# Performance work log

Measured on AMD Instinct MI355X. Metric: run time of the kernel, lower is better.

The kernel has to match this reference:

```python
import jax, jax.numpy as jnp
import numpy as np

D_MODEL = 1024
N_HEADS = 16
D_K = D_MODEL // N_HEADS
D_FF = 4096
EPS = 1e-5


def _layer_norm(x, gamma, beta):
    mu = jnp.mean(x, axis=-1, keepdims=True)
    var = jnp.var(x, axis=-1, keepdims=True)
    return (x - mu) * jax.lax.rsqrt(var + EPS) * gamma + beta


def setup_inputs() -> dict:
    key = jax.random.key(0)
    ks = jax.random.split(key, 16)
    s = 1.0 / np.sqrt(D_MODEL)
    sf = 1.0 / np.sqrt(D_FF)
    return {
        "x": jax.random.normal(ks[0], (2, 2048, D_MODEL), dtype=jnp.float32),
        "Wq": jax.random.uniform(ks[1], (D_MODEL, D_MODEL), minval=-s, maxval=s),
        "bq": jax.random.uniform(ks[2], (D_MODEL,), minval=-s, maxval=s),
        "Wk": jax.random.uniform(ks[3], (D_MODEL, D_MODEL), minval=-s, maxval=s),
        "bk": jax.random.uniform(ks[4], (D_MODEL,), minval=-s, maxval=s),
        "Wv": jax.random.uniform(ks[5], (D_MODEL, D_MODEL), minval=-s, maxval=s),
        "bv": jax.random.uniform(ks[6], (D_MODEL,), minval=-s, maxval=s),
        "Wo": jax.random.uniform(ks[7], (D_MODEL, D_MODEL), minval=-s, maxval=s),
        "bo": jax.random.uniform(ks[8], (D_MODEL,), minval=-s, maxval=s),
        "W1": jax.random.uniform(ks[9], (D_MODEL, D_FF), minval=-s, maxval=s),
        "b1": jax.random.uniform(ks[10], (D_FF,), minval=-s, maxval=s),
        "W2": jax.random.uniform(ks[11], (D_FF, D_MODEL), minval=-sf, maxval=sf),
        "b2": jax.random.uniform(ks[12], (D_MODEL,), minval=-sf, maxval=sf),
        "g1": jnp.ones((D_MODEL,)),
        "be1": jnp.zeros((D_MODEL,)),
        "g2": jnp.ones((D_MODEL,)),
        "be2": jnp.zeros((D_MODEL,)),
    }


def reference(x, Wq, bq, Wk, bk, Wv, bv, Wo, bo, W1, b1, W2, b2, g1, be1, g2, be2):
    B, S, _ = x.shape

    def heads(y):  # (B,S,D) -> (B,H,S,dk)
        return y.reshape(B, S, N_HEADS, D_K).transpose(0, 2, 1, 3)

    q = heads(x @ Wq + bq)
    k = heads(x @ Wk + bk)
    v = heads(x @ Wv + bv)

    scores = jnp.einsum("bhqd,bhkd->bhqk", q, k) / np.sqrt(D_K)
    attn = jax.nn.softmax(scores, axis=-1)
    out = jnp.einsum("bhqk,bhkd->bhqd", attn, v)
    out = out.transpose(0, 2, 1, 3).reshape(B, S, D_MODEL)
    attn_out = out @ Wo + bo

    resid_mid = _layer_norm(x + attn_out, g1, be1)
    ff = jnp.maximum(resid_mid @ W1 + b1, 0.0) @ W2 + b2
    return _layer_norm(resid_mid + ff, g2, be2)
```

## Files before the change

### kernel.cpp

```cpp
#include <hip/hip_runtime.h>

#define DM   1024
#define DFF  4096
#define NH   16
#define DKH  64
#define SEQ  2048
#define BATCH 2
#define ROWS (BATCH*SEQ)
#define QKS  2048

typedef __bf16 bf16x8 __attribute__((ext_vector_type(8)));
typedef float  f32x4  __attribute__((ext_vector_type(4)));

__device__ __forceinline__ unsigned short f2b(float f) {
    unsigned int u = __builtin_bit_cast(unsigned int, f);
    u += 0x7fffu + ((u >> 16) & 1u);
    return (unsigned short)(u >> 16);
}
__device__ __forceinline__ float b2f(unsigned short u) {
    return __builtin_bit_cast(float, (unsigned int)u << 16);
}
__device__ __forceinline__ float exp2_raw(float x) {
    float r;
    asm("v_exp_f32 %0, %1" : "=v"(r) : "v"(x));
    return r;
}

__device__ __forceinline__ void gl_lds16(const unsigned short* g, unsigned short* l) {
    __builtin_amdgcn_global_load_lds(
        (const __attribute__((address_space(1))) unsigned int*)(const void*)g,
        (__attribute__((address_space(3))) unsigned int*)(void*)l, 16, 0, 0);
}

__global__ __launch_bounds__(256) void k_prep(const float* __restrict__ x,
                                              const float* __restrict__ Wq,
                                              const float* __restrict__ Wk,
                                              const float* __restrict__ Wv,
                                              const float* __restrict__ Wo,
                                              const float* __restrict__ W1,
                                              const float* __restrict__ W2,
                                              unsigned short* __restrict__ xb,
                                              unsigned short* __restrict__ WqkT,
                                              unsigned short* __restrict__ WvT,
                                              unsigned short* __restrict__ WoT,
                                              unsigned short* __restrict__ W1T,
                                              unsigned short* __restrict__ W2T) {
    int z = blockIdx.z;
    int bid = blockIdx.y * gridDim.x + blockIdx.x;
    int tx = threadIdx.x, ty = threadIdx.y;
    if (z == 6) {
        int i = bid * 256 + ty * 32 + tx;
        float4 v = ((const float4*)x)[i];
        ushort4 u;
        u.x = f2b(v.x); u.y = f2b(v.y); u.z = f2b(v.z); u.w = f2b(v.w);
        ((ushort4*)xb)[i] = u;
        return;
    }
    const float* W; unsigned short* WT; int R, C;
    if      (z == 0) { W = Wq; WT = WqkT;                     R = DM;  C = DM;  }
    else if (z == 1) { W = Wk; WT = WqkT + (size_t)DM * DM;   R = DM;  C = DM;  }
    else if (z == 2) { W = Wv; WT = WvT;                      R = DM;  C = DM;  }
    else if (z == 3) { W = Wo; WT = WoT;                      R = DM;  C = DM;  }
    else if (z == 4) { W = W1; WT = W1T;                      R = DM;  C = DFF; }
    else             { W = W2; WT = W2T;                      R = DFF; C = DM;  }
    int ct = C / 32;
    if (bid >= (R / 32) * ct) return;
    int c0 = (bid % ct) * 32, r0 = (bid / ct) * 32;
    __shared__ float t[32][33];
#pragma unroll
    for (int i = 0; i < 4; i++) {
        int r = ty + i * 8;
        t[r][tx] = W[(size_t)(r0 + r) * C + c0 + tx];
    }
    __syncthreads();
#pragma unroll
    for (int i = 0; i < 4; i++) {
        int r = ty + i * 8;
        WT[(size_t)(c0 + r) * R + r0 + tx] = f2b(t[tx][r]);
    }
}

template<int WM, int WN, bool OUTF32, bool RELU, bool BIASROW, bool VPERM, bool SCALE2, bool SPLITK, bool SUPER2D>
__global__ __launch_bounds__(256) void k_gemm_bt(const unsigned short* __restrict__ A,
                                                 const unsigned short* __restrict__ BT,
                                                 const float* __restrict__ bias,
                                                 const float* __restrict__ bias2,
                                                 int bsplit, float sc2,
                                                 void* __restrict__ Cout,
                                                 int M, int N, int K) {
    constexpr int BM = 2 * WM, BN = 2 * WN;
    constexpr int MT = WM / 16, NT = WN / 16;
    constexpr int IA = BM / 32, IB = BN / 32;
    __shared__ unsigned short As[BM][64] __attribute__((aligned(16)));
    __shared__ unsigned short Bs[BN][64] __attribute__((aligned(16)));
    int tid = threadIdx.x;
    int w = tid >> 6, l = tid & 63;
    int wr = w >> 1, wc = w & 1;
    int l15 = l & 15, lg = l >> 4;

    int bid = blockIdx.y * gridDim.x + blockIdx.x;
    int nwg = gridDim.x * gridDim.y;
    int m0, n0;
    if (SUPER2D) {
        int xcd = bid & 7, q = bid >> 3;
        int RM = gridDim.y >> 1, RN = gridDim.x >> 2;
        int mI = (xcd >> 2) * RM + (q % RM);
        int nI = (xcd & 3) * RN + (q / RM);
        m0 = mI * BM; n0 = nI * BN;
    } else {
        int swz = (bid & 7) * (nwg >> 3) + (bid >> 3);
        m0 = (swz / gridDim.x) * BM; n0 = (swz % gridDim.x) * BN;
    }

    int kb_ = SPLITK ? (int)blockIdx.z * (K >> 1) : 0;
    int Keff = SPLITK ? (K >> 1) : K;

    int lr8 = l >> 3;
    int gsrc = (l & 7) ^ lr8;
    const unsigned short* Abase = A  + (size_t)(m0 + w * (BM / 4) + lr8) * K + kb_ + gsrc * 8;
    const unsigned short* Bbase = BT + (size_t)(n0 + w * (BN / 4) + lr8) * K + kb_ + gsrc * 8;

    f32x4 acc[MT][NT] = {};

    int nk = Keff >> 6;
    for (int kt = 0; kt < nk; ++kt) {
        __syncthreads();
#pragma unroll
        for (int it = 0; it < IA; ++it)
            gl_lds16(Abase + (size_t)(it * 8) * K + kt * 64, &As[w * (BM / 4) + it * 8][0]);
#pragma unroll
        for (int it = 0; it < IB; ++it)
            gl_lds16(Bbase + (size_t)(it * 8) * K + kt * 64, &Bs[w * (BN / 4) + it * 8][0]);
        __syncthreads();
#pragma unroll
        for (int ks = 0; ks < 2; ++ks) {
            int glog = ks * 4 + lg;
            bf16x8 af[MT], bfr[NT];
#pragma unroll
            for (int mt = 0; mt < MT; ++mt) {
                int row = wr * WM + mt * 16 + l15;
                af[mt] = *(const bf16x8*)&As[row][(glog ^ (row & 7)) << 3];
            }
#pragma unroll
            for (int nt = 0; nt < NT; ++nt) {
                int row = wc * WN + nt * 16 + l15;
                bfr[nt] = *(const bf16x8*)&Bs[row][(glog ^ (row & 7)) << 3];
            }
#pragma unroll
            for (int mt = 0; mt < MT; ++mt)
#pragma unroll
                for (int nt = 0; nt < NT; ++nt)
                    acc[mt][nt] = __builtin_amdgcn_mfma_f32_16x16x32_bf16(af[mt], bfr[nt], acc[mt][nt], 0, 0, 0);
        }
    }
    float*          CoutF = (float*)Cout          + (SPLITK ? (size_t)blockIdx.z * M * N : 0);
    unsigned short* CoutH = (unsigned short*)Cout + (SPLITK ? (size_t)blockIdx.z * M * N : 0);
    float browv[MT][4];
    if (BIASROW) {
#pragma unroll
        for (int mt = 0; mt < MT; ++mt)
#pragma unroll
            for (int r = 0; r < 4; ++r)
                browv[mt][r] = bias[m0 + wr * WM + mt * 16 + lg * 4 + r];
    }
#pragma unroll
    for (int nt = 0; nt < NT; ++nt) {
        int colo = VPERM ? (32 * (nt >> 1) + 4 * (nt & 1) + 8 * (l15 >> 2) + (l15 & 3))
                         : (nt * 16 + l15);
        int col = n0 + wc * WN + colo;
        float bv = BIASROW ? 0.f : (col < bsplit ? bias[col] : bias2[col - bsplit]);
        if (SPLITK && blockIdx.z != 0) bv = 0.f;
#pragma unroll
        for (int mt = 0; mt < MT; ++mt) {
#pragma unroll
            for (int r = 0; r < 4; ++r) {
                int row = m0 + wr * WM + mt * 16 + lg * 4 + r;
                float v = acc[mt][nt][r] + (BIASROW ? browv[mt][r] : bv);
                if (SCALE2 && col >= bsplit) v *= sc2;
                if (RELU) v = fmaxf(v, 0.f);
                if (OUTF32) CoutF[(size_t)row * N + col] = v;
                else        CoutH[(size_t)row * N + col] = f2b(v);
            }
        }
    }
}

__global__ __launch_bounds__(512) void k_attn(const unsigned short* __restrict__ Q,
                                              const unsigned short* __restrict__ Kb,
                                              const unsigned short* __restrict__ VT,
                                              unsigned short* __restrict__ O) {
    __shared__ unsigned short ksA[64][64] __attribute__((aligned(16)));
    __shared__ unsigned short vsA[64][64] __attribute__((aligned(16)));
    __shared__ unsigned short ksB[64][64] __attribute__((aligned(16)));
    __shared__ unsigned short vsB[64][64] __attribute__((aligned(16)));

    int tid = threadIdx.x;
    int w = tid >> 6, l = tid & 63;
    int l15 = l & 15, lg = l >> 4;

    int bid = blockIdx.y * gridDim.x + blockIdx.x;
    int bh = (bid & 7) * 4 + ((bid >> 3) & 3);
    int qt = bid >> 5;
    int b = bh >> 4, h = bh & 15;
    int row0 = qt * 128;

    const unsigned short* qg  = Q  + (size_t)b * SEQ * QKS + h * DKH;
    const unsigned short* kg  = Kb + (size_t)b * SEQ * QKS + h * DKH;
    const unsigned short* vtg = VT + (size_t)(h * DKH) * ROWS + (size_t)b * SEQ;

    int lr8 = l >> 3;
    int gsrc = (l & 7) ^ lr8;

    const unsigned short* kp0 = kg  + (size_t)(w * 8 + lr8) * QKS + gsrc * 8;
    const unsigned short* vp0 = vtg + (size_t)(w * 8 + lr8) * ROWS + gsrc * 8;

    gl_lds16(kp0, &ksA[w * 8][0]);
    gl_lds16(vp0, &vsA[w * 8][0]);
    kp0 += (size_t)64 * QKS; vp0 += 64;

    bf16x8 aq[2];
    {
        int qrow = row0 + w * 16 + l15;
        aq[0] = *(const bf16x8*)(qg + (size_t)qrow * QKS + lg * 8);
        aq[1] = *(const bf16x8*)(qg + (size_t)qrow * QKS + (4 + lg) * 8);
    }

    int dsoff[2][4];
#pragma unroll
    for (int ksi = 0; ksi < 2; ksi++)
#pragma unroll
        for (int nt = 0; nt < 4; nt++) {
            int row = nt * 16 + l15;
            int glog = ksi * 4 + lg;
            dsoff[ksi][nt] = row * 128 + ((glog ^ (row & 7)) << 4);
        }

    union { bf16x8 v; unsigned int u[4]; } ones;
#pragma unroll
    for (int i = 0; i < 4; i++) ones.u[i] = 0x3f803f80u;

    f32x4 o[4] = {};
    f32x4 osum = {};

    __syncthreads();

    auto body = [&](unsigned short (&kbuf)[64][64], unsigned short (&vbuf)[64][64],
                    unsigned short (&knext)[64][64], unsigned short (&vnext)[64][64],
                    bool doStage) {
        if (doStage) {
            gl_lds16(kp0, &knext[w * 8][0]);
            gl_lds16(vp0, &vnext[w * 8][0]);
            kp0 += (size_t)64 * QKS; vp0 += 64;
        }

        f32x4 s[4] = {};
        __builtin_amdgcn_s_setprio(1);
#pragma unroll
        for (int ksi = 0; ksi < 2; ksi++)
#pragma unroll
            for (int nt = 0; nt < 4; nt++) {
                bf16x8 bk = *(const bf16x8*)((const char*)&kbuf[0][0] + dsoff[ksi][nt]);
                s[nt] = __builtin_amdgcn_mfma_f32_16x16x32_bf16(bk, aq[ksi], s[nt], 0, 0, 0);
            }
        __builtin_amdgcn_s_setprio(0);

        union { bf16x8 v; unsigned int u[4]; } A0, A1;
#pragma unroll
        for (int nt = 0; nt < 4; nt++)
#pragma unroll
            for (int w2 = 0; w2 < 2; w2++) {
                float e0 = exp2_raw(s[nt][2 * w2]);
                float e1 = exp2_raw(s[nt][2 * w2 + 1]);
                unsigned int pk;
                asm("v_cvt_pk_bf16_f32 %0, %1, %2" : "=v"(pk) : "v"(e0), "v"(e1));
                if (nt < 2) A0.u[(nt & 1) * 2 + w2] = pk;
                else        A1.u[(nt & 1) * 2 + w2] = pk;
            }

        __builtin_amdgcn_s_setprio(1);
        osum = __builtin_amdgcn_mfma_f32_16x16x32_bf16(A0.v, ones.v, osum, 0, 0, 0);
        osum = __builtin_amdgcn_mfma_f32_16x16x32_bf16(A1.v, ones.v, osum, 0, 0, 0);
#pragma unroll
        for (int ksi = 0; ksi < 2; ksi++)
#pragma unroll
            for (int nt = 0; nt < 4; nt++) {
                bf16x8 bv = *(const bf16x8*)((const char*)&vbuf[0][0] + dsoff[ksi][nt]);
                o[nt] = __builtin_amdgcn_mfma_f32_16x16x32_bf16(ksi == 0 ? A0.v : A1.v, bv, o[nt], 0, 0, 0);
            }
        __builtin_amdgcn_s_setprio(0);

        __syncthreads();
    };

    for (int kt2 = 0; kt2 < 16; ++kt2) {
        body(ksA, vsA, ksB, vsB, true);
        body(ksB, vsB, ksA, vsA, kt2 < 15);
    }

    float rinv[4];
#pragma unroll
    for (int r = 0; r < 4; r++) rinv[r] = 1.f / osum[r];

    unsigned short* og = O + (size_t)b * SEQ * DM + h * DKH;
#pragma unroll
    for (int nt = 0; nt < 4; nt++) {
        int d = nt * 16 + l15;
#pragma unroll
        for (int r = 0; r < 4; r++) {
            int srow_ = row0 + w * 16 + lg * 4 + r;
            og[(size_t)srow_ * DM + d] = f2b(o[nt][r] * rinv[r]);
        }
    }
}

template<bool WB16, bool ADD3, bool BC16>
__global__ __launch_bounds__(256) void k_add_ln(const float* __restrict__ a,
                                                const void* __restrict__ b,
                                                const void* __restrict__ c,
                                                const float* __restrict__ gamma,
                                                const float* __restrict__ beta,
                                                float* __restrict__ outf,
                                                unsigned short* __restrict__ outb) {
    __shared__ float red[8];
    int row = blockIdx.x, tid = threadIdx.x;
    float4 va = ((const float4*)(a + (size_t)row * DM))[tid];
    float4 vb, vc;
    if (BC16) {
        ushort4 ub = ((const ushort4*)((const unsigned short*)b + (size_t)row * DM))[tid];
        vb.x = b2f(ub.x); vb.y = b2f(ub.y); vb.z = b2f(ub.z); vb.w = b2f(ub.w);
    } else {
        vb = ((const float4*)((const float*)b + (size_t)row * DM))[tid];
    }
    float4 v;
    v.x = va.x + vb.x; v.y = va.y + vb.y; v.z = va.z + vb.z; v.w = va.w + vb.w;
    if (ADD3) {
        if (BC16) {
            ushort4 uc = ((const ushort4*)((const unsigned short*)c + (size_t)row * DM))[tid];
            vc.x = b2f(uc.x); vc.y = b2f(uc.y); vc.z = b2f(uc.z); vc.w = b2f(uc.w);
        } else {
            vc = ((const float4*)((const float*)c + (size_t)row * DM))[tid];
        }
        v.x += vc.x; v.y += vc.y; v.z += vc.z; v.w += vc.w;
    }
    float s = v.x + v.y + v.z + v.w;
    float q = v.x * v.x + v.y * v.y + v.z * v.z + v.w * v.w;
#pragma unroll
    for (int m = 1; m < 64; m <<= 1) { s += __shfl_xor(s, m); q += __shfl_xor(q, m); }
    if ((tid & 63) == 0) { red[tid >> 6] = s; red[4 + (tid >> 6)] = q; }
    __syncthreads();
    float tot  = red[0] + red[1] + red[2] + red[3];
    float totq = red[4] + red[5] + red[6] + red[7];
    float mu = tot * (1.f / DM);
    float var = totq * (1.f / DM) - mu * mu;
    float rs = rsqrtf(var + 1e-5f);
    float4 g  = ((const float4*)gamma)[tid];
    float4 be = ((const float4*)beta)[tid];
    float4 y;
    y.x = (v.x - mu) * rs * g.x + be.x;
    y.y = (v.y - mu) * rs * g.y + be.y;
    y.z = (v.z - mu) * rs * g.z + be.z;
    y.w = (v.w - mu) * rs * g.w + be.w;
    ((float4*)(outf + (size_t)row * DM))[tid] = y;
    if (WB16) {
        ushort4 u;
        u.x = f2b(y.x); u.y = f2b(y.y); u.z = f2b(y.z); u.w = f2b(y.w);
        ((ushort4*)(outb + (size_t)row * DM))[tid] = u;
    }
}

extern "C" void kernel_launch(void* const* d_in, const int* in_sizes, int n_in,
                              void* d_out, int out_size, void* d_ws, size_t ws_size,
                              hipStream_t stream) {
    const float* x   = (const float*)d_in[0];
    const float* Wq  = (const float*)d_in[1];
    const float* bq  = (const float*)d_in[2];
    const float* Wk  = (const float*)d_in[3];
    const float* bk  = (const float*)d_in[4];
    const float* Wv  = (const float*)d_in[5];
    const float* bv  = (const float*)d_in[6];
    const float* Wo  = (const float*)d_in[7];
    const float* bo  = (const float*)d_in[8];
    const float* W1  = (const float*)d_in[9];
    const float* b1  = (const float*)d_in[10];
    const float* W2  = (const float*)d_in[11];
    const float* b2  = (const float*)d_in[12];
    const float* g1  = (const float*)d_in[13];
    const float* be1 = (const float*)d_in[14];
    const float* g2  = (const float*)d_in[15];
    const float* be2 = (const float*)d_in[16];

    char* ws = (char*)d_ws;
    const size_t MB = 1u << 20;
    unsigned short* xb    = (unsigned short*)(ws + 0);
    unsigned short* WqkT  = (unsigned short*)(ws + 8 * MB);
    unsigned short* WvT   = (unsigned short*)(ws + 12 * MB);
    unsigned short* WoT   = (unsigned short*)(ws + 14 * MB);
    unsigned short* W1T   = (unsigned short*)(ws + 16 * MB);
    unsigned short* W2T   = (unsigned short*)(ws + 24 * MB);
    unsigned short* qkb   = (unsigned short*)(ws + 32 * MB);
    unsigned short* vT    = (unsigned short*)(ws + 48 * MB);
    unsigned short* prtb  = (unsigned short*)(ws + 32 * MB);
    float*          resid = (float*)(ws + 72 * MB);
    unsigned short* residb= (unsigned short*)(ws + 88 * MB);
    unsigned short* h1    = (unsigned short*)(ws + 96 * MB);

    dim3 blk(256);
    const int BIG = 1 << 30;
    const float SC = 0.125f * 1.44269504f;

    k_prep<<<dim3(128, 32, 7), dim3(32, 8), 0, stream>>>(x, Wq, Wk, Wv, Wo, W1, W2,
                                                         xb, WqkT, WvT, WoT, W1T, W2T);

    k_gemm_bt<32, 64, false, false, false, false, true, false, false><<<dim3(QKS / 128, ROWS / 64), blk, 0, stream>>>(
        xb, WqkT, bq, bk, DM, SC, qkb, ROWS, QKS, DM);
    k_gemm_bt<32, 64, false, false, true, true, false, false, false><<<dim3(ROWS / 128, DM / 64), blk, 0, stream>>>(
        WvT, xb, bv, bv, BIG, 1.f, vT, DM, ROWS, DM);

    k_attn<<<dim3(SEQ / 128, BATCH * NH), dim3(512), 0, stream>>>(qkb, qkb + DM, vT, xb);

    k_gemm_bt<32, 64, false, false, false, false, false, true, false><<<dim3(DM / 128, ROWS / 64, 2), blk, 0, stream>>>(
        xb, WoT, bo, bo, BIG, 1.f, prtb, ROWS, DM, DM);
    k_add_ln<true, true, true><<<ROWS, blk, 0, stream>>>(x, prtb, prtb + (size_t)ROWS * DM, g1, be1, resid, residb);

    k_gemm_bt<64, 64, false, true, false, false, false, false, true><<<dim3(DFF / 128, ROWS / 128), blk, 0, stream>>>(
        residb, W1T, b1, b1, BIG, 1.f, h1, ROWS, DFF, DM);
    k_gemm_bt<32, 64, false, false, false, false, false, true, false><<<dim3(DM / 128, ROWS / 64, 2), blk, 0, stream>>>(
        h1, W2T, b2, b2, BIG, 1.f, prtb, ROWS, DM, DFF);
    k_add_ln<false, true, true><<<ROWS, blk, 0, stream>>>(resid, prtb, prtb + (size_t)ROWS * DM, g2, be2, (float*)d_out, nullptr);
}
```

Before: 226.1 us.

## Fuse QK and V projections into one launch; drop fp32 residual copy

The separate QK and V projection GEMM launches are merged into a single kernel with 1536 blocks. Blocks below 1024 compute the QK output and the rest compute the transposed V, so the two GEMMs share one launch and fill the GPU together. The first layer norm no longer writes an fp32 residual. The final layer norm reads the bf16 residual instead, which cuts memory traffic but rounds the residual path to bf16 and may reduce accuracy.

New measurement: 216.6 us. -4.2%, faster.

```diff
diff --git a/kernel.cpp b/kernel.cpp
--- a/kernel.cpp
+++ b/kernel.cpp
@@ -185,6 +185,115 @@
     }
 }
 
+__global__ __launch_bounds__(256) void k_gemm_qkv(const unsigned short* __restrict__ xb,
+                                                  const unsigned short* __restrict__ WqkT,
+                                                  const unsigned short* __restrict__ WvT,
+                                                  const float* __restrict__ bq,
+                                                  const float* __restrict__ bk,
+                                                  const float* __restrict__ bv,
+                                                  float sc,
+                                                  unsigned short* __restrict__ qkb,
+                                                  unsigned short* __restrict__ vT) {
+    constexpr int BM = 64, BN = 128, MT = 2, NT = 4, IA = 2, IB = 4;
+    const int K = DM;
+    __shared__ unsigned short As[BM][64] __attribute__((aligned(16)));
+    __shared__ unsigned short Bs[BN][64] __attribute__((aligned(16)));
+    int tid = threadIdx.x;
+    int w = tid >> 6, l = tid & 63;
+    int wr = w >> 1, wc = w & 1;
+    int l15 = l & 15, lg = l >> 4;
+
+    int bid1 = blockIdx.x;
+    bool isQK = bid1 < 1024;
+    const unsigned short *A, *BT;
+    int m0, n0;
+    if (isQK) {
+        int bid = bid1;
+        int swz = (bid & 7) * 128 + (bid >> 3);
+        m0 = (swz / 16) * BM; n0 = (swz % 16) * BN;
+        A = xb; BT = WqkT;
+    } else {
+        int bid = bid1 - 1024;
+        int swz = (bid & 7) * 64 + (bid >> 3);
+        m0 = (swz / 32) * BM; n0 = (swz % 32) * BN;
+        A = WvT; BT = xb;
+    }
+
+    int lr8 = l >> 3;
+    int gsrc = (l & 7) ^ lr8;
+    const unsigned short* Abase = A  + (size_t)(m0 + w * (BM / 4) + lr8) * K + gsrc * 8;
+    const unsigned short* Bbase = BT + (size_t)(n0 + w * (BN / 4) + lr8) * K + gsrc * 8;
+
+    f32x4 acc[MT][NT] = {};
+
+    for (int kt = 0; kt < K / 64; ++kt) {
+        __syncthreads();
+#pragma unroll
+        for (int it = 0; it < IA; ++it)
+            gl_lds16(Abase + (size_t)(it * 8) * K + kt * 64, &As[w * (BM / 4) + it * 8][0]);
+#pragma unroll
+        for (int it = 0; it < IB; ++it)
+            gl_lds16(Bbase + (size_t)(it * 8) * K + kt * 64, &Bs[w * (BN / 4) + it * 8][0]);
+        __syncthreads();
+#pragma unroll
+        for (int ks = 0; ks < 2; ++ks) {
+            int glog = ks * 4 + lg;
+            bf16x8 af[MT], bfr[NT];
+#pragma unroll
+            for (int mt = 0; mt < MT; ++mt) {
+                int row = wr * 32 + mt * 16 + l15;
+                af[mt] = *(const bf16x8*)&As[row][(glog ^ (row & 7)) << 3];
+            }
+#pragma unroll
+            for (int nt = 0; nt < NT; ++nt) {
+                int row = wc * 64 + nt * 16 + l15;
+                bfr[nt] = *(const bf16x8*)&Bs[row][(glog ^ (row & 7)) << 3];
+            }
+#pragma unroll
+            for (int mt = 0; mt < MT; ++mt)
+#pragma unroll
+                for (int nt = 0; nt < NT; ++nt)
+                    acc[mt][nt] = __builtin_amdgcn_mfma_f32_16x16x32_bf16(af[mt], bfr[nt], acc[mt][nt], 0, 0, 0);
+        }
+    }
+
+    if (isQK) {
+#pragma unroll
+        for (int nt = 0; nt < NT; ++nt) {
+            int col = n0 + wc * 64 + nt * 16 + l15;
+            float bvx = col < DM ? bq[col] : bk[col - DM];
+#pragma unroll
+            for (int mt = 0; mt < MT; ++mt)
+#pragma unroll
+                for (int r = 0; r < 4; ++r) {
+                    int row = m0 + wr * 32 + mt * 16 + lg * 4 + r;
+                    float v = acc[mt][nt][r] + bvx;
+                    if (col >= DM) v *= sc;
+                    qkb[(size_t)row * QKS + col] = f2b(v);
+                }
+        }
+    } else {
+        float browv[MT][4];
+#pragma unroll
+        for (int mt = 0; mt < MT; ++mt)
+#pragma unroll
+            for (int r = 0; r < 4; ++r)
+                browv[mt][r] = bv[m0 + wr * 32 + mt * 16 + lg * 4 + r];
+#pragma unroll
+        for (int nt = 0; nt < NT; ++nt) {
+            int colo = 32 * (nt >> 1) + 4 * (nt & 1) + 8 * (l15 >> 2) + (l15 & 3);
+            int col = n0 + wc * 64 + colo;
+#pragma unroll
+            for (int mt = 0; mt < MT; ++mt)
+#pragma unroll
+                for (int r = 0; r < 4; ++r) {
+                    int row = m0 + wr * 32 + mt * 16 + lg * 4 + r;
+                    vT[(size_t)row * ROWS + col] = f2b(acc[mt][nt][r] + browv[mt][r]);
+                }
+        }
+    }
+}
+
 __global__ __launch_bounds__(512) void k_attn(const unsigned short* __restrict__ Q,
                                               const unsigned short* __restrict__ Kb,
                                               const unsigned short* __restrict__ VT,
@@ -313,8 +422,8 @@
     }
 }
 
-template<bool WB16, bool ADD3, bool BC16>
-__global__ __launch_bounds__(256) void k_add_ln(const float* __restrict__ a,
+template<bool A16, bool WF32, bool WB16, bool ADD3, bool BC16>
+__global__ __launch_bounds__(256) void k_add_ln(const void* __restrict__ a,
                                                 const void* __restrict__ b,
                                                 const void* __restrict__ c,
                                                 const float* __restrict__ gamma,
@@ -323,7 +432,13 @@
                                                 unsigned short* __restrict__ outb) {
     __shared__ float red[8];
     int row = blockIdx.x, tid = threadIdx.x;
-    float4 va = ((const float4*)(a + (size_t)row * DM))[tid];
+    float4 va;
+    if (A16) {
+        ushort4 ua = ((const ushort4*)((const unsigned short*)a + (size_t)row * DM))[tid];
+        va.x = b2f(ua.x); va.y = b2f(ua.y); va.z = b2f(ua.z); va.w = b2f(ua.w);
+    } else {
+        va = ((const float4*)((const float*)a + (size_t)row * DM))[tid];
+    }
     float4 vb, vc;
     if (BC16) {
         ushort4 ub = ((const ushort4*)((const unsigned short*)b + (size_t)row * DM))[tid];
@@ -360,7 +475,7 @@
     y.y = (v.y - mu) * rs * g.y + be.y;
     y.z = (v.z - mu) * rs * g.z + be.z;
     y.w = (v.w - mu) * rs * g.w + be.w;
-    ((float4*)(outf + (size_t)row * DM))[tid] = y;
+    if (WF32) ((float4*)(outf + (size_t)row * DM))[tid] = y;
     if (WB16) {
         ushort4 u;
         u.x = f2b(y.x); u.y = f2b(y.y); u.z = f2b(y.z); u.w = f2b(y.w);
@@ -400,7 +515,6 @@
     unsigned short* qkb   = (unsigned short*)(ws + 32 * MB);
     unsigned short* vT    = (unsigned short*)(ws + 48 * MB);
     unsigned short* prtb  = (unsigned short*)(ws + 32 * MB);
-    float*          resid = (float*)(ws + 72 * MB);
     unsigned short* residb= (unsigned short*)(ws + 88 * MB);
     unsigned short* h1    = (unsigned short*)(ws + 96 * MB);
 
@@ -411,20 +525,19 @@
     k_prep<<<dim3(128, 32, 7), dim3(32, 8), 0, stream>>>(x, Wq, Wk, Wv, Wo, W1, W2,
                                                          xb, WqkT, WvT, WoT, W1T, W2T);
 
-    k_gemm_bt<32, 64, false, false, false, false, true, false, false><<<dim3(QKS / 128, ROWS / 64), blk, 0, stream>>>(
-        xb, WqkT, bq, bk, DM, SC, qkb, ROWS, QKS, DM);
-    k_gemm_bt<32, 64, false, false, true, true, false, false, false><<<dim3(ROWS / 128, DM / 64), blk, 0, stream>>>(
-        WvT, xb, bv, bv, BIG, 1.f, vT, DM, ROWS, DM);
+    k_gemm_qkv<<<dim3(1536), blk, 0, stream>>>(xb, WqkT, WvT, bq, bk, bv, SC, qkb, vT);
 
     k_attn<<<dim3(SEQ / 128, BATCH * NH), dim3(512), 0, stream>>>(qkb, qkb + DM, vT, xb);
 
     k_gemm_bt<32, 64, false, false, false, false, false, true, false><<<dim3(DM / 128, ROWS / 64, 2), blk, 0, stream>>>(
         xb, WoT, bo, bo, BIG, 1.f, prtb, ROWS, DM, DM);
-    k_add_ln<true, true, true><<<ROWS, blk, 0, stream>>>(x, prtb, prtb + (size_t)ROWS * DM, g1, be1, resid, residb);
+    k_add_ln<false, false, true, true, true><<<ROWS, blk, 0, stream>>>(
+        x, prtb, prtb + (size_t)ROWS * DM, g1, be1, nullptr, residb);
 
     k_gemm_bt<64, 64, false, true, false, false, false, false, true><<<dim3(DFF / 128, ROWS / 128), blk, 0, stream>>>(
         residb, W1T, b1, b1, BIG, 1.f, h1, ROWS, DFF, DM);
     k_gemm_bt<32, 64, false, false, false, false, false, true, false><<<dim3(DM / 128, ROWS / 64, 2), blk, 0, stream>>>(
         h1, W2T, b2, b2, BIG, 1.f, prtb, ROWS, DM, DFF);
-    k_add_ln<false, true, true><<<ROWS, blk, 0, stream>>>(resid, prtb, prtb + (size_t)ROWS * DM, g2, be2, (float*)d_out, nullptr);
-}
+    k_add_ln<true, true, false, true, true><<<ROWS, blk, 0, stream>>>(
+        residb, prtb, prtb + (size_t)ROWS * DM, g2, be2, (float*)d_out, nullptr);
+}
```
